# Performance work log

Hardware: AMD Instinct MI355X
Metric: run time of the kernel (lower is better)

Reference implementation:

```python
import jax, jax.numpy as jnp
import numpy as np

N_NODES = 100000
N_EDGES = 3200000
D_IN = 128
D_HID = 128
N_CLASSES = 40


def setup_inputs() -> dict:
    key = jax.random.key(0)
    ks = jax.random.split(key, 8)
    x = jax.random.normal(ks[0], (N_NODES, D_IN), dtype=jnp.float32)
    edge_index = jax.random.randint(ks[1], (2, N_EDGES), 0, N_NODES, dtype=jnp.int64)
    s1 = 1.0 / np.sqrt(D_IN)
    s2 = 1.0 / np.sqrt(D_HID)
    W1 = jax.random.normal(ks[2], (D_IN, D_HID), dtype=jnp.float32) * s1
    b1 = jnp.zeros((D_HID,), dtype=jnp.float32)
    W2 = jax.random.normal(ks[3], (D_HID, D_HID), dtype=jnp.float32) * s2
    b2 = jnp.zeros((D_HID,), dtype=jnp.float32)
    Wl = jax.random.normal(ks[4], (D_HID, N_CLASSES), dtype=jnp.float32) * s2
    bl = jnp.zeros((N_CLASSES,), dtype=jnp.float32)
    return {"x": x, "edge_index": edge_index, "W1": W1, "b1": b1,
            "W2": W2, "b2": b2, "Wl": Wl, "bl": bl}


def _gcn_conv(x, W, b, src, dst, inv_sqrt_deg, n_nodes):
    # h = X @ W  (linear transform first: cheaper when out_dim <= in_dim)
    h = x @ W  # [N, d_out]
    # symmetric normalization: norm_e = deg(src)^-1/2 * deg(dst)^-1/2
    norm = inv_sqrt_deg[src] * inv_sqrt_deg[dst]  # [E]
    msg = h[src] * norm[:, None]                  # gather + scale  [E, d_out]
    out = jax.ops.segment_sum(msg, dst, num_segments=n_nodes)  # scatter-add
    return out + b


def reference(x, edge_index, W1, b1, W2, b2, Wl, bl):
    n = x.shape[0]
    # GCNConv adds self-loops before normalization (PyG default)
    loops = jnp.arange(n, dtype=edge_index.dtype)
    src = jnp.concatenate([edge_index[0], loops])
    dst = jnp.concatenate([edge_index[1], loops])
    deg = jax.ops.segment_sum(jnp.ones_like(dst, dtype=x.dtype), dst, num_segments=n)
    inv_sqrt_deg = jnp.where(deg > 0, jax.lax.rsqrt(deg), 0.0)

    h = _gcn_conv(x, W1, b1, src, dst, inv_sqrt_deg, n)
    h = jax.nn.relu(h)
    h = _gcn_conv(h, W2, b2, src, dst, inv_sqrt_deg, n)
    h = jax.nn.relu(h)
    return h @ Wl + bl
```

## Files before the change

kernel.cpp:

```cpp
#include <hip/hip_runtime.h>
#include <hip/hip_bf16.h>

typedef _Float16 f16;
typedef _Float16 f16x8 __attribute__((ext_vector_type(8)));

#define D 128
#define N_CLS 40
#define BN 128
#define NBMAX 1024

__global__ __launch_bounds__(256) void k_hist(const int* __restrict__ dst,
                                              int* __restrict__ bcnt, int e) {
  __shared__ int lh[NBMAX];
  for (int j = threadIdx.x; j < NBMAX; j += 256) lh[j] = 0;
  __syncthreads();
  int stride = gridDim.x * blockDim.x;
  for (int q = blockIdx.x * blockDim.x + threadIdx.x; q < e; q += stride)
    atomicAdd(&lh[dst[q] >> 7], 1);
  __syncthreads();
  for (int j = threadIdx.x; j < NBMAX; j += 256)
    if (lh[j]) atomicAdd(&bcnt[j], lh[j]);
}

__global__ __launch_bounds__(1024) void k_bscan(const int* __restrict__ bcnt,
                                                int* __restrict__ bbase,
                                                int* __restrict__ bcur) {
  __shared__ int sums[NBMAX];
  int t = threadIdx.x;
  int c = bcnt[t];
  sums[t] = c;
  __syncthreads();
  for (int off = 1; off < NBMAX; off <<= 1) {
    int a = (t >= off) ? sums[t - off] : 0;
    __syncthreads();
    sums[t] += a;
    __syncthreads();
  }
  bbase[t] = sums[t] - c;
  bcur[t] = sums[t] - c;
}

__global__ __launch_bounds__(256) void k_place(const int* __restrict__ src,
                                               const int* __restrict__ dst,
                                               int* __restrict__ bcur,
                                               unsigned int* __restrict__ binned,
                                               int e, int nwg) {
  __shared__ int lh[NBMAX];
  __shared__ int lofs[NBMAX];
  __shared__ int lcur[NBMAX];
  int chunk = (e + nwg - 1) / nwg;
  int lo = blockIdx.x * chunk;
  int hi = min(e, lo + chunk);
  int t = threadIdx.x;
  for (int j = t; j < NBMAX; j += 256) { lh[j] = 0; lcur[j] = 0; }
  __syncthreads();
  for (int q = lo + t; q < hi; q += 256) atomicAdd(&lh[dst[q] >> 7], 1);
  __syncthreads();
  for (int j = t; j < NBMAX; j += 256) {
    int c = lh[j];
    lofs[j] = c ? atomicAdd(&bcur[j], c) : 0;
  }
  __syncthreads();
  for (int q = lo + t; q < hi; q += 256) {
    int d = dst[q];
    int b = d >> 7;
    int r = atomicAdd(&lcur[b], 1);
    binned[lofs[b] + r] = ((unsigned int)(d & 127) << 17) | (unsigned int)src[q];
  }
}

__global__ __launch_bounds__(256) void k_csr(const unsigned int* __restrict__ binned,
                                             const int* __restrict__ bbase,
                                             int* __restrict__ csr,
                                             int* __restrict__ deg,
                                             float* __restrict__ isd,
                                             int* __restrict__ row_start, int n) {
  int b = blockIdx.x;
  int lo = bbase[b], hi = bbase[b + 1];
  __shared__ int h[BN];
  __shared__ int sc[BN];
  __shared__ int cur[BN];
  int t = threadIdx.x;
  if (t < BN) h[t] = 0;
  __syncthreads();
  for (int q = lo + t; q < hi; q += 256) atomicAdd(&h[binned[q] >> 17], 1);
  __syncthreads();
  if (t < BN) sc[t] = h[t];
  __syncthreads();
  for (int off = 1; off < BN; off <<= 1) {
    int a = 0;
    if (t < BN && t >= off) a = sc[t - off];
    __syncthreads();
    if (t < BN) sc[t] += a;
    __syncthreads();
  }
  if (t < BN) {
    int excl = sc[t] - h[t];
    cur[t] = lo + excl;
    int i = b * BN + t;
    if (i < n) {
      deg[i] = h[t];
      isd[i] = rsqrtf((float)(h[t] + 1));
      row_start[i] = lo + excl;
    }
  }
  __syncthreads();
  for (int q = lo + t; q < hi; q += 256) {
    unsigned int u = binned[q];
    int p = atomicAdd(&cur[u >> 17], 1);
    csr[p] = (int)(u & 0x1FFFF);
  }
}

template <bool HALF_IN>
__global__ __launch_bounds__(256) void k_gemm_t(const void* __restrict__ Xv,
                                                const float* __restrict__ W,
                                                const float* __restrict__ isd,
                                                f16* __restrict__ HS, int n) {
  __shared__ float Xt[64][D + 4];
  __shared__ float Wb[32][D + 4];
  int t = threadIdx.x;
  int r0 = blockIdx.x * 64;
  if (!HALF_IN) {
    const float* X = (const float*)Xv;
    for (int q = t; q < 64 * 32; q += 256) {
      int row = q >> 5, cb = (q & 31) << 2;
      float4 v = {0.f, 0.f, 0.f, 0.f};
      if (r0 + row < n) v = *(const float4*)(X + (size_t)(r0 + row) * D + cb);
      *(float4*)&Xt[row][cb] = v;
    }
  } else {
    const f16* X = (const f16*)Xv;
    for (int q = t; q < 64 * 16; q += 256) {
      int row = q >> 4, cb = (q & 15) << 3;
      f16x8 v = 0;
      if (r0 + row < n) v = *(const f16x8*)(X + (size_t)(r0 + row) * D + cb);
      float* xp = &Xt[row][cb];
#pragma unroll
      for (int j = 0; j < 8; ++j) xp[j] = (float)v[j];
    }
  }
  int tr = ((t >> 4) & 15) << 2;
  int tc = (t & 15) << 3;
  float acc[4][8];
#pragma unroll
  for (int i = 0; i < 4; ++i)
#pragma unroll
    for (int j = 0; j < 8; ++j) acc[i][j] = 0.f;

  for (int hh = 0; hh < 4; ++hh) {
    __syncthreads();
    for (int q = t; q < 32 * 32; q += 256) {
      int row = q >> 5, cb = (q & 31) << 2;
      *(float4*)&Wb[row][cb] = *(const float4*)(W + (size_t)(hh * 32 + row) * D + cb);
    }
    __syncthreads();
#pragma unroll 4
    for (int k = 0; k < 32; ++k) {
      float4 u0 = *(const float4*)&Wb[k][tc];
      float4 u1 = *(const float4*)&Wb[k][tc + 4];
      float bv[8] = {u0.x, u0.y, u0.z, u0.w, u1.x, u1.y, u1.z, u1.w};
      int kk = hh * 32 + k;
#pragma unroll
      for (int i = 0; i < 4; ++i) {
        float a = Xt[tr + i][kk];
#pragma unroll
        for (int j = 0; j < 8; ++j) acc[i][j] += a * bv[j];
      }
    }
  }
#pragma unroll
  for (int i = 0; i < 4; ++i) {
    int row = r0 + tr + i;
    if (row < n) {
      float s = isd[row];
      f16x8 ov;
#pragma unroll
      for (int j = 0; j < 8; ++j) ov[j] = (f16)(s * acc[i][j]);
      *(f16x8*)(HS + (size_t)row * D + tc) = ov;
    }
  }
}

__device__ inline void gather8(const f16* __restrict__ HS,
                               const int* __restrict__ csr,
                               int start, int c, int lane, float acc[8]) {
  int g = lane >> 4;
  int l = lane & 15;
  const char* base = (const char*)HS;
  size_t lofs = (size_t)(l << 4);
#pragma unroll
  for (int j = 0; j < 8; ++j) acc[j] = 0.f;

  for (int e0 = 0; e0 < c; e0 += 64) {
    int nb = min(64, c - e0);
    int idx = (lane < nb) ? csr[start + e0 + lane] : 0;
    int kb = 0;
    for (; kb + 16 <= nb; kb += 16) {
      f16x8 a16 = 0;
#pragma unroll
      for (int k = 0; k < 16; k += 4) {
        int s = __shfl(idx, kb + k + g);
        a16 += *(const f16x8*)(base + (((size_t)s) << 8) + lofs);
      }
#pragma unroll
      for (int j = 0; j < 8; ++j) acc[j] += (float)a16[j];
    }
    if (kb < nb) {
      f16x8 a16 = 0;
      for (int k = kb; k < nb; k += 4) {
        int kk = k + g;
        int s = __shfl(idx, kk);
        f16x8 u = *(const f16x8*)(base + (((size_t)s) << 8) + lofs);
        if (kk < nb) a16 += u;
      }
#pragma unroll
      for (int j = 0; j < 8; ++j) acc[j] += (float)a16[j];
    }
  }
#pragma unroll
  for (int j = 0; j < 8; ++j) {
    float v = acc[j];
    v += __shfl_xor(v, 16);
    v += __shfl_xor(v, 32);
    acc[j] = v;
  }
}

__global__ __launch_bounds__(64) void k_agg1(const f16* __restrict__ HS,
                                             const int* __restrict__ csr,
                                             const int* __restrict__ row_start,
                                             const int* __restrict__ deg,
                                             const float* __restrict__ isd,
                                             const float* __restrict__ bias,
                                             f16* __restrict__ G) {
  int i = blockIdx.x;
  int lane = threadIdx.x;
  int l = lane & 15;
  float acc[8];
  gather8(HS, csr, row_start[i], deg[i], lane, acc);
  f16x8 sv = *(const f16x8*)(HS + (size_t)i * D + l * 8);
  float di = isd[i];
  float4 bb0 = *(const float4*)(bias + l * 8);
  float4 bb1 = *(const float4*)(bias + l * 8 + 4);
  float bv[8] = {bb0.x, bb0.y, bb0.z, bb0.w, bb1.x, bb1.y, bb1.z, bb1.w};
  f16x8 ov;
#pragma unroll
  for (int j = 0; j < 8; ++j) {
    float v = di * (acc[j] + (float)sv[j]) + bv[j];
    v = v > 0.f ? v : 0.f;
    ov[j] = (f16)v;
  }
  if ((lane >> 4) == 0) *(f16x8*)(G + (size_t)i * D + l * 8) = ov;
}

__global__ __launch_bounds__(64) void k_agg_cls(const f16* __restrict__ HS,
                                                const int* __restrict__ csr,
                                                const int* __restrict__ row_start,
                                                const int* __restrict__ deg,
                                                const float* __restrict__ isd,
                                                const float* __restrict__ b2,
                                                const float* __restrict__ Wl,
                                                const float* __restrict__ bl,
                                                float* __restrict__ out) {
  int i = blockIdx.x;
  int lane = threadIdx.x;
  int l = lane & 15;
  float acc[8];
  gather8(HS, csr, row_start[i], deg[i], lane, acc);
  f16x8 sv = *(const f16x8*)(HS + (size_t)i * D + l * 8);
  float di = isd[i];
  float4 bb0 = *(const float4*)(b2 + l * 8);
  float4 bb1 = *(const float4*)(b2 + l * 8 + 4);
  float bv[8] = {bb0.x, bb0.y, bb0.z, bb0.w, bb1.x, bb1.y, bb1.z, bb1.w};
  __shared__ float tt[D];
#pragma unroll
  for (int j = 0; j < 8; ++j) {
    float v = di * (acc[j] + (float)sv[j]) + bv[j];
    bv[j] = v > 0.f ? v : 0.f;
  }
  if ((lane >> 4) == 0) {
    *(float4*)&tt[l * 8] = make_float4(bv[0], bv[1], bv[2], bv[3]);
    *(float4*)&tt[l * 8 + 4] = make_float4(bv[4], bv[5], bv[6], bv[7]);
  }
  __syncthreads();
  if (lane < N_CLS) {
    float o = bl[lane];
#pragma unroll 8
    for (int k = 0; k < D; ++k) o += tt[k] * Wl[k * N_CLS + lane];
    out[(size_t)i * N_CLS + lane] = o;
  }
}

extern "C" void kernel_launch(void* const* d_in, const int* in_sizes, int n_in,
                              void* d_out, int out_size, void* d_ws, size_t ws_size,
                              hipStream_t stream) {
  const float* x  = (const float*)d_in[0];
  const int*   ei = (const int*)d_in[1];
  const float* W1 = (const float*)d_in[2];
  const float* b1 = (const float*)d_in[3];
  const float* W2 = (const float*)d_in[4];
  const float* b2 = (const float*)d_in[5];
  const float* Wl = (const float*)d_in[6];
  const float* bl = (const float*)d_in[7];
  float* out = (float*)d_out;

  const int n = in_sizes[0] / D;
  const int e = in_sizes[1] / 2;
  const int* src = ei;
  const int* dst = ei + e;
  const int nb = (n + BN - 1) / BN;

  char* ws = (char*)d_ws;
  size_t off = 0;
  auto alloc = [&](size_t bytes) -> void* {
    void* p = ws + off;
    off += (bytes + 255) & ~(size_t)255;
    return p;
  };
  int*   bcnt      = (int*)alloc(NBMAX * 4);
  int*   bbase     = (int*)alloc(NBMAX * 4);
  int*   bcur      = (int*)alloc(NBMAX * 4);
  int*   deg       = (int*)alloc((size_t)n * 4);
  int*   row_start = (int*)alloc((size_t)n * 4);
  float* isd       = (float*)alloc((size_t)n * 4);
  int*   csr       = (int*)alloc((size_t)e * 4);
  f16*   hA        = (f16*)alloc((size_t)n * D * 2);
  f16*   hB        = (f16*)alloc((size_t)n * D * 2);
  unsigned int* binned = (unsigned int*)hA;

  hipMemsetAsync(bcnt, 0, NBMAX * 4, stream);

  const int nwg_place = 512;
  k_hist<<<1024, 256, 0, stream>>>(dst, bcnt, e);
  k_bscan<<<1, 1024, 0, stream>>>(bcnt, bbase, bcur);
  k_place<<<nwg_place, 256, 0, stream>>>(src, dst, bcur, binned, e, nwg_place);
  k_csr<<<nb, 256, 0, stream>>>(binned, bbase, csr, deg, isd, row_start, n);

  int gblocks = (n + 63) / 64;
  k_gemm_t<false><<<gblocks, 256, 0, stream>>>(x, W1, isd, hA, n);
  k_agg1<<<n, 64, 0, stream>>>(hA, csr, row_start, deg, isd, b1, hB);
  k_gemm_t<true><<<gblocks, 256, 0, stream>>>(hB, W2, isd, hA, n);
  k_agg_cls<<<n, 64, 0, stream>>>(hA, csr, row_start, deg, isd, b2, Wl, bl, out);
}
```

Baseline: 576.3 us.

## Slice feature matrix into column panels for cache-local gathers; split classifier

The hidden-feature buffers are now stored as 8 column slices of 16 halves each, and aggregation launches one 64-lane block per (node, slice). Each slice's gathered rows come from a smaller region of memory, which is meant to keep the random neighbor gathers resident in L2/MALL. The classifier matmul is moved out of the aggregation kernel into a separate tiled GEMM kernel. The cost is 8x more blocks, 8x more CSR index reads, and an extra kernel launch plus a round trip of the layer-2 output through memory.

```diff
diff --git a/kernel.cpp b/kernel.cpp
--- a/kernel.cpp
+++ b/kernel.cpp
@@ -3,11 +3,14 @@
 
 typedef _Float16 f16;
 typedef _Float16 f16x8 __attribute__((ext_vector_type(8)));
+typedef _Float16 f16x4 __attribute__((ext_vector_type(4)));
 
 #define D 128
 #define N_CLS 40
 #define BN 128
 #define NBMAX 1024
+#define NSLICE 8
+#define SW 16
 
 __global__ __launch_bounds__(256) void k_hist(const int* __restrict__ dst,
                                               int* __restrict__ bcnt, int e) {
@@ -134,7 +137,9 @@
     for (int q = t; q < 64 * 16; q += 256) {
       int row = q >> 4, cb = (q & 15) << 3;
       f16x8 v = 0;
-      if (r0 + row < n) v = *(const f16x8*)(X + (size_t)(r0 + row) * D + cb);
+      if (r0 + row < n)
+        v = *(const f16x8*)(X + (size_t)(cb >> 4) * n * SW +
+                            ((size_t)(r0 + row) << 4) + (cb & 8));
       float* xp = &Xt[row][cb];
 #pragma unroll
       for (int j = 0; j < 8; ++j) xp[j] = (float)v[j];
@@ -177,118 +182,116 @@
       f16x8 ov;
 #pragma unroll
       for (int j = 0; j < 8; ++j) ov[j] = (f16)(s * acc[i][j]);
-      *(f16x8*)(HS + (size_t)row * D + tc) = ov;
-    }
-  }
-}
-
-__device__ inline void gather8(const f16* __restrict__ HS,
-                               const int* __restrict__ csr,
-                               int start, int c, int lane, float acc[8]) {
-  int g = lane >> 4;
-  int l = lane & 15;
-  const char* base = (const char*)HS;
-  size_t lofs = (size_t)(l << 4);
-#pragma unroll
-  for (int j = 0; j < 8; ++j) acc[j] = 0.f;
-
-  for (int e0 = 0; e0 < c; e0 += 64) {
-    int nb = min(64, c - e0);
-    int idx = (lane < nb) ? csr[start + e0 + lane] : 0;
-    int kb = 0;
-    for (; kb + 16 <= nb; kb += 16) {
-      f16x8 a16 = 0;
-#pragma unroll
-      for (int k = 0; k < 16; k += 4) {
-        int s = __shfl(idx, kb + k + g);
-        a16 += *(const f16x8*)(base + (((size_t)s) << 8) + lofs);
-      }
-#pragma unroll
-      for (int j = 0; j < 8; ++j) acc[j] += (float)a16[j];
-    }
-    if (kb < nb) {
-      f16x8 a16 = 0;
-      for (int k = kb; k < nb; k += 4) {
-        int kk = k + g;
-        int s = __shfl(idx, kk);
-        f16x8 u = *(const f16x8*)(base + (((size_t)s) << 8) + lofs);
-        if (kk < nb) a16 += u;
-      }
-#pragma unroll
-      for (int j = 0; j < 8; ++j) acc[j] += (float)a16[j];
-    }
-  }
-#pragma unroll
-  for (int j = 0; j < 8; ++j) {
-    float v = acc[j];
-    v += __shfl_xor(v, 16);
-    v += __shfl_xor(v, 32);
-    acc[j] = v;
-  }
-}
-
-__global__ __launch_bounds__(64) void k_agg1(const f16* __restrict__ HS,
+      *(f16x8*)(HS + (size_t)(tc >> 4) * n * SW + ((size_t)row << 4) + (tc & 8)) = ov;
+    }
+  }
+}
+
+__global__ __launch_bounds__(64) void k_aggs(const f16* __restrict__ IN,
                                              const int* __restrict__ csr,
                                              const int* __restrict__ row_start,
                                              const int* __restrict__ deg,
                                              const float* __restrict__ isd,
                                              const float* __restrict__ bias,
-                                             f16* __restrict__ G) {
-  int i = blockIdx.x;
+                                             f16* __restrict__ OUT, int n) {
+  int s = blockIdx.x & 7;
+  int i = blockIdx.x >> 3;
   int lane = threadIdx.x;
-  int l = lane & 15;
-  float acc[8];
-  gather8(HS, csr, row_start[i], deg[i], lane, acc);
-  f16x8 sv = *(const f16x8*)(HS + (size_t)i * D + l * 8);
+  int sub = lane >> 2;
+  int q = lane & 3;
+  const f16* T = IN + (size_t)s * n * SW;
+  int c = deg[i];
+  int start = row_start[i];
+  float fa0 = 0.f, fa1 = 0.f, fa2 = 0.f, fa3 = 0.f;
+  for (int e0 = 0; e0 < c; e0 += 64) {
+    int nb = min(64, c - e0);
+    int idx = (lane < nb) ? __builtin_nontemporal_load(&csr[start + e0 + lane]) : 0;
+    int full = nb >> 4;
+    f16x4 a0 = 0, a1 = 0;
+    int blk = 0;
+    for (; blk + 2 <= full; blk += 2) {
+      int s0 = __shfl(idx, (blk << 4) + sub);
+      int s1 = __shfl(idx, ((blk + 1) << 4) + sub);
+      f16x4 u0 = *(const f16x4*)(T + ((size_t)s0 << 4) + (q << 2));
+      f16x4 u1 = *(const f16x4*)(T + ((size_t)s1 << 4) + (q << 2));
+      a0 += u0;
+      a1 += u1;
+    }
+    if (blk < full) {
+      int s0 = __shfl(idx, (blk << 4) + sub);
+      a0 += *(const f16x4*)(T + ((size_t)s0 << 4) + (q << 2));
+    }
+    int k = (full << 4) + sub;
+    {
+      int s0 = __shfl(idx, k < nb ? k : 0);
+      f16x4 u = *(const f16x4*)(T + ((size_t)s0 << 4) + (q << 2));
+      if (k < nb) a1 += u;
+    }
+    fa0 += (float)a0[0] + (float)a1[0];
+    fa1 += (float)a0[1] + (float)a1[1];
+    fa2 += (float)a0[2] + (float)a1[2];
+    fa3 += (float)a0[3] + (float)a1[3];
+  }
+#pragma unroll
+  for (int m = 4; m <= 32; m <<= 1) {
+    fa0 += __shfl_xor(fa0, m);
+    fa1 += __shfl_xor(fa1, m);
+    fa2 += __shfl_xor(fa2, m);
+    fa3 += __shfl_xor(fa3, m);
+  }
+  f16x4 sv = *(const f16x4*)(T + ((size_t)i << 4) + (q << 2));
   float di = isd[i];
-  float4 bb0 = *(const float4*)(bias + l * 8);
-  float4 bb1 = *(const float4*)(bias + l * 8 + 4);
-  float bv[8] = {bb0.x, bb0.y, bb0.z, bb0.w, bb1.x, bb1.y, bb1.z, bb1.w};
-  f16x8 ov;
-#pragma unroll
-  for (int j = 0; j < 8; ++j) {
-    float v = di * (acc[j] + (float)sv[j]) + bv[j];
-    v = v > 0.f ? v : 0.f;
-    ov[j] = (f16)v;
-  }
-  if ((lane >> 4) == 0) *(f16x8*)(G + (size_t)i * D + l * 8) = ov;
-}
-
-__global__ __launch_bounds__(64) void k_agg_cls(const f16* __restrict__ HS,
-                                                const int* __restrict__ csr,
-                                                const int* __restrict__ row_start,
-                                                const int* __restrict__ deg,
-                                                const float* __restrict__ isd,
-                                                const float* __restrict__ b2,
-                                                const float* __restrict__ Wl,
-                                                const float* __restrict__ bl,
-                                                float* __restrict__ out) {
-  int i = blockIdx.x;
-  int lane = threadIdx.x;
-  int l = lane & 15;
-  float acc[8];
-  gather8(HS, csr, row_start[i], deg[i], lane, acc);
-  f16x8 sv = *(const f16x8*)(HS + (size_t)i * D + l * 8);
-  float di = isd[i];
-  float4 bb0 = *(const float4*)(b2 + l * 8);
-  float4 bb1 = *(const float4*)(b2 + l * 8 + 4);
-  float bv[8] = {bb0.x, bb0.y, bb0.z, bb0.w, bb1.x, bb1.y, bb1.z, bb1.w};
-  __shared__ float tt[D];
-#pragma unroll
-  for (int j = 0; j < 8; ++j) {
-    float v = di * (acc[j] + (float)sv[j]) + bv[j];
-    bv[j] = v > 0.f ? v : 0.f;
-  }
-  if ((lane >> 4) == 0) {
-    *(float4*)&tt[l * 8] = make_float4(bv[0], bv[1], bv[2], bv[3]);
-    *(float4*)&tt[l * 8 + 4] = make_float4(bv[4], bv[5], bv[6], bv[7]);
-  }
-  __syncthreads();
-  if (lane < N_CLS) {
-    float o = bl[lane];
-#pragma unroll 8
-    for (int k = 0; k < D; ++k) o += tt[k] * Wl[k * N_CLS + lane];
-    out[(size_t)i * N_CLS + lane] = o;
+  float4 bb = *(const float4*)(bias + s * SW + (q << 2));
+  float v0 = di * (fa0 + (float)sv[0]) + bb.x;
+  float v1 = di * (fa1 + (float)sv[1]) + bb.y;
+  float v2 = di * (fa2 + (float)sv[2]) + bb.z;
+  float v3 = di * (fa3 + (float)sv[3]) + bb.w;
+  f16x4 ov;
+  ov[0] = (f16)(v0 > 0.f ? v0 : 0.f);
+  ov[1] = (f16)(v1 > 0.f ? v1 : 0.f);
+  ov[2] = (f16)(v2 > 0.f ? v2 : 0.f);
+  ov[3] = (f16)(v3 > 0.f ? v3 : 0.f);
+  if (lane < 4)
+    *(f16x4*)(OUT + (size_t)s * n * SW + ((size_t)i << 4) + (q << 2)) = ov;
+}
+
+__global__ __launch_bounds__(256) void k_cls(const f16* __restrict__ T,
+                                             const float* __restrict__ Wl,
+                                             const float* __restrict__ bl,
+                                             float* __restrict__ out, int n) {
+  __shared__ float Xt[64][D + 4];
+  __shared__ float Wb[D][N_CLS + 8];
+  int t = threadIdx.x;
+  int r0 = blockIdx.x * 64;
+  for (int chunk = t; chunk < 64 * 16; chunk += 256) {
+    int row = chunk >> 4, cb = (chunk & 15) << 3;
+    f16x8 v = 0;
+    if (r0 + row < n)
+      v = *(const f16x8*)(T + (size_t)(cb >> 4) * n * SW +
+                          ((size_t)(r0 + row) << 4) + (cb & 8));
+    float* xp = &Xt[row][cb];
+#pragma unroll
+    for (int j = 0; j < 8; ++j) xp[j] = (float)v[j];
+  }
+  for (int q2 = t; q2 < D * N_CLS; q2 += 256) {
+    int k = q2 / N_CLS, o = q2 - k * N_CLS;
+    Wb[k][o] = Wl[q2];
+  }
+  __syncthreads();
+  int row = t >> 2;
+  int cg = t & 3;
+  float acc[10];
+#pragma unroll
+  for (int j = 0; j < 10; ++j) acc[j] = bl[cg * 10 + j];
+  for (int k = 0; k < D; ++k) {
+    float xv = Xt[row][k];
+#pragma unroll
+    for (int j = 0; j < 10; ++j) acc[j] += xv * Wb[k][cg * 10 + j];
+  }
+  if (r0 + row < n) {
+    float* op = out + (size_t)(r0 + row) * N_CLS + cg * 10;
+#pragma unroll
+    for (int j = 0; j < 10; ++j) op[j] = acc[j];
   }
 }
 
@@ -339,7 +342,8 @@
 
   int gblocks = (n + 63) / 64;
   k_gemm_t<false><<<gblocks, 256, 0, stream>>>(x, W1, isd, hA, n);
-  k_agg1<<<n, 64, 0, stream>>>(hA, csr, row_start, deg, isd, b1, hB);
+  k_aggs<<<n * NSLICE, 64, 0, stream>>>(hA, csr, row_start, deg, isd, b1, hB, n);
   k_gemm_t<true><<<gblocks, 256, 0, stream>>>(hB, W2, isd, hA, n);
-  k_agg_cls<<<n, 64, 0, stream>>>(hA, csr, row_start, deg, isd, b2, Wl, bl, out);
-}
+  k_aggs<<<n * NSLICE, 64, 0, stream>>>(hA, csr, row_start, deg, isd, b2, hB, n);
+  k_cls<<<gblocks, 256, 0, stream>>>(hB, Wl, bl, out, n);
+}
```

After: 943.9 us. 63.8% more time.
